# Optimization experiments

Measured on AMD Instinct MI355X. Metric: run time of the kernel, lower is better.

The kernel has to match this reference:

```python
import jax, jax.numpy as jnp
import numpy as np

N = 50000
SELF_LOOP_W = 2.0  # GCNConv(improved=True)


def gcn_conv(x, edge_index, W, b):
    # x: [N, Fin], edge_index: [2, E] (row=source, col=target)
    h = x @ W  # [N, Fout]
    row, col = edge_index[0], edge_index[1]
    ones = jnp.ones(row.shape[0], dtype=h.dtype)
    deg = jax.ops.segment_sum(ones, col, num_segments=N) + SELF_LOOP_W
    dinv = jnp.where(deg > 0, jax.lax.rsqrt(deg), 0.0)
    norm = dinv[row] * dinv[col]  # [E]
    agg = jax.ops.segment_sum(norm[:, None] * h[row], col, num_segments=N)
    # self-loop contribution: weight 2.0, norm = dinv[i]^2
    agg = agg + (SELF_LOOP_W * dinv * dinv)[:, None] * h
    return agg + b


def setup_inputs() -> dict:
    key = jax.random.key(0)
    ks = jax.random.split(key, 12)
    F_in, H1, H2, H3 = 256, 256, 128, 64
    E, Ep, En = 800000, 200000, 200000
    def glorot(k, shape):
        lim = np.sqrt(6.0 / (shape[0] + shape[1]))
        return jax.random.uniform(k, shape, jnp.float32, -lim, lim)
    return {
        "x": jax.random.normal(ks[0], (N, F_in), jnp.float32),
        "train_edge_index": jax.random.randint(ks[1], (2, E), 0, N),
        "pos_edge_index": jax.random.randint(ks[2], (2, Ep), 0, N),
        "neg_edge_index": jax.random.randint(ks[3], (2, En), 0, N),
        "W1": glorot(ks[4], (F_in, H1)),
        "b1": jnp.zeros((H1,), jnp.float32),
        "W2": glorot(ks[5], (H1, H2)),
        "b2": jnp.zeros((H2,), jnp.float32),
        "Wl1": glorot(ks[6], (H2, H3)),
        "bl1": jnp.zeros((H3,), jnp.float32),
        "Wl2": glorot(ks[7], (H3, 1)),
        "bl2": jnp.zeros((1,), jnp.float32),
    }


def reference(x, train_edge_index, pos_edge_index, neg_edge_index,
              W1, b1, W2, b2, Wl1, bl1, Wl2, bl2):
    h = jax.nn.relu(gcn_conv(x, train_edge_index, W1, b1))
    h = gcn_conv(h, train_edge_index, W2, b2)  # [N, 128]
    tei = jnp.concatenate([pos_edge_index, neg_edge_index], axis=-1)  # [2, Ep+En]
    e = h[tei[1]] + h[tei[0]]  # x_i + x_j, [Etot, 128]
    e = jax.nn.relu(e @ Wl1 + bl1)
    e = jax.nn.sigmoid(e @ Wl2 + bl2)
    return e.reshape(-1)
```

## Files before the change

### kernel.cpp

```cpp
#include <hip/hip_runtime.h>
#include <math.h>

#define NV 50000
#define ETR 800000
#define EPOS 200000
#define ETEST 400000

typedef __attribute__((ext_vector_type(8))) short bf16x8;
typedef __attribute__((ext_vector_type(8))) unsigned short ushortx8;
typedef __attribute__((ext_vector_type(4))) float f32x4;

__device__ inline unsigned short f2b(float f) {
    union { float f; unsigned u; } v; v.f = f;
    unsigned r = v.u + 0x7fffu + ((v.u >> 16) & 1u);
    return (unsigned short)(r >> 16);
}
__device__ inline float blo(unsigned q) { union { unsigned u; float f; } v; v.u = q << 16; return v.f; }
__device__ inline float bhi(unsigned q) { union { unsigned u; float f; } v; v.u = q & 0xffff0000u; return v.f; }
__device__ inline float b2f(unsigned short s) { union { unsigned u; float f; } v; v.u = ((unsigned)s) << 16; return v.f; }

#define GLOAD_LDS16(g, l) __builtin_amdgcn_global_load_lds( \
    (__attribute__((address_space(1))) void*)(g), \
    (__attribute__((address_space(3))) void*)(l), 16, 0, 0)


template<int N, int K, bool AF32, int NCOLS = N>
__device__ __forceinline__ void gemm_body(
    const void* __restrict__ Av, const unsigned short* __restrict__ Bt,
    unsigned short* __restrict__ C, int M, int row0, int col0)
{
    constexpr int BK = 64;
    __shared__ unsigned short smem[18464];
    unsigned short (*Asm)[BK] = (unsigned short (*)[BK])smem;
    unsigned short (*Bsm)[BK] = (unsigned short (*)[BK])(smem + 8192);
    int tid = threadIdx.x;
    int lane = tid & 63, wid = tid >> 6;
    int wr = wid >> 1, wc = wid & 1;

    int sr = tid >> 3;
    int s8 = tid & 7;
    int fr = lane & 15;
    int g  = lane >> 4;

    f32x4 acc[4][4] = {};

    for (int k0 = 0; k0 < K; k0 += BK) {
        #pragma unroll
        for (int i = 0; i < 4; ++i) {
            int r = sr + i * 32;
            int gr = row0 + r;
            int s8sw = s8 ^ (r & 7);
            GLOAD_LDS16(&Bt[(size_t)(col0 + r) * K + k0 + s8sw * 8], &Bsm[r][s8 * 8]);
            if constexpr (AF32) {
                const float* Af = (const float*)Av;
                ushortx8 va = {0, 0, 0, 0, 0, 0, 0, 0};
                if (gr < M) {
                    float4 f0 = *(const float4*)&Af[(size_t)gr * K + k0 + s8 * 8];
                    float4 f1 = *(const float4*)&Af[(size_t)gr * K + k0 + s8 * 8 + 4];
                    va[0] = f2b(f0.x); va[1] = f2b(f0.y); va[2] = f2b(f0.z); va[3] = f2b(f0.w);
                    va[4] = f2b(f1.x); va[5] = f2b(f1.y); va[6] = f2b(f1.z); va[7] = f2b(f1.w);
                }
                *(ushortx8*)&Asm[r][(s8 ^ (r & 7)) * 8] = va;
            } else {
                const unsigned short* Ab = (const unsigned short*)Av;
                GLOAD_LDS16(&Ab[(size_t)gr * K + k0 + s8sw * 8], &Asm[r][s8 * 8]);
            }
        }
        __syncthreads();
        #pragma unroll
        for (int kf = 0; kf < BK; kf += 32) {
            int sbase = kf >> 3;
            bf16x8 af[4], bfr[4];
            #pragma unroll
            for (int m = 0; m < 4; ++m) {
                int rr = wr * 64 + m * 16 + fr;
                af[m] = *(const bf16x8*)&Asm[rr][((sbase + g) ^ (fr & 7)) * 8];
            }
            #pragma unroll
            for (int n = 0; n < 4; ++n) {
                int rr = wc * 64 + n * 16 + fr;
                bfr[n] = *(const bf16x8*)&Bsm[rr][((sbase + g) ^ (fr & 7)) * 8];
            }
            #pragma unroll
            for (int m = 0; m < 4; ++m)
                #pragma unroll
                for (int n = 0; n < 4; ++n)
                    acc[m][n] = __builtin_amdgcn_mfma_f32_16x16x32_bf16(af[m], bfr[n], acc[m][n], 0, 0, 0);
        }
        __syncthreads();
    }

    {
        unsigned short* cw = smem + wid * 4616;
        #pragma unroll
        for (int m = 0; m < 4; ++m)
            #pragma unroll
            for (int n = 0; n < 4; ++n)
                #pragma unroll
                for (int j = 0; j < 4; ++j)
                    cw[(m * 16 + g * 4 + j) * 72 + n * 16 + fr] = f2b(acc[m][n][j]);
        __syncthreads();
        int row = tid >> 1;
        int half = tid & 1;
        int q = ((row >> 6) << 1) + half;
        int rl = row & 63;
        const unsigned short* cr = smem + q * 4616 + rl * 72;
        int gr = row0 + row;
        if (gr < M && half * 64 < NCOLS) {
            unsigned short* gp = C + (size_t)gr * NCOLS + col0 + half * 64;
            #pragma unroll
            for (int c8 = 0; c8 < 8; ++c8)
                *(ushortx8*)&gp[c8 * 8] = *(const ushortx8*)&cr[c8 * 8];
        }
    }
}


__global__ __launch_bounds__(256) void fat0_kernel(
    const int* __restrict__ tei, int* __restrict__ deg,
    const float* __restrict__ W1, unsigned short* __restrict__ w1t)
{
    int bid = blockIdx.x;
    int t = threadIdx.x;
    if (bid < 3125) {
        int e = bid * 256 + t;
        if (e < ETR) atomicAdd(&deg[tei[ETR + e]], 1);
    } else {
        int i = (bid - 3125) * 256 + t;
        w1t[i] = f2b(W1[(i & 255) * 256 + (i >> 8)]);
    }
}


__global__ __launch_bounds__(1024) void ptr2_kernel(
    const int* __restrict__ deg, int* __restrict__ ptr,
    int* __restrict__ cursor, float* __restrict__ dinv)
{
    int b = blockIdx.x, t = threadIdx.x;
    int lane = t & 63, w = t >> 6;
    __shared__ int wred[16], wsum[16], woff[16];
    __shared__ int base_s;

    int pre = 0;
    int lim = b * 1024;
    for (int i = t; i < lim; i += 1024) pre += deg[i];
    #pragma unroll
    for (int off = 32; off > 0; off >>= 1) pre += __shfl_xor(pre, off);
    if (lane == 0) wred[w] = pre;
    __syncthreads();
    if (t == 0) {
        int s = 0;
        #pragma unroll
        for (int k = 0; k < 16; ++k) s += wred[k];
        base_s = s;
    }

    int i = b * 1024 + t;
    int d = (i < NV) ? deg[i] : 0;
    int v = d;
    #pragma unroll
    for (int off = 1; off < 64; off <<= 1) {
        int u = __shfl_up(v, off);
        if (lane >= off) v += u;
    }
    if (lane == 63) wsum[w] = v;
    __syncthreads();
    if (t == 0) {
        int s = base_s;
        #pragma unroll
        for (int k = 0; k < 16; ++k) { woff[k] = s; s += wsum[k]; }
    }
    __syncthreads();
    int excl = woff[w] + v - d;
    if (i < NV) {
        ptr[i] = excl;
        cursor[i] = excl;
        dinv[i] = rsqrtf((float)d + 2.0f);
        if (i == NV - 1) ptr[NV] = excl + d;
    }
}


__global__ __launch_bounds__(256) void fat1_kernel(
    const float* __restrict__ x, const unsigned short* __restrict__ w1t,
    unsigned short* __restrict__ h1lin,
    const int* __restrict__ tei, const float* __restrict__ dinv,
    int* __restrict__ cursor, int2* __restrict__ edat,
    const float* __restrict__ W2, unsigned short* __restrict__ w2t,
    const float* __restrict__ Wl1, unsigned short* __restrict__ wl1t)
{
    int bid = blockIdx.x;
    int t = threadIdx.x;
    if (bid < 782) {
        int row0 = (bid >> 1) * 128, col0 = (bid & 1) * 128;
        gemm_body<256, 256, true>(x, w1t, h1lin, NV, row0, col0);
    } else if (bid < 3907) {
        int e = (bid - 782) * 256 + t;
        if (e < ETR) {
            int row = tei[e];
            int col = tei[ETR + e];
            int p = atomicAdd(&cursor[col], 1);
            edat[p] = make_int2(row, __float_as_int(dinv[row] * dinv[col]));
        }
    } else if (bid < 4035) {
        int i = (bid - 3907) * 256 + t;
        w2t[i] = f2b(W2[(i & 255) * 128 + (i >> 8)]);
    } else if (bid < 4067) {
        int i = (bid - 4035) * 256 + t;
        wl1t[i] = f2b(Wl1[(i & 127) * 64 + (i >> 7)]);
    } else {
        int i = (bid - 4067) * 256 + t;
        wl1t[8192 + i] = 0;
    }
}


__global__ __launch_bounds__(256) void gemm2_kernel(
    const unsigned short* __restrict__ A, const unsigned short* __restrict__ Bt,
    unsigned short* __restrict__ C)
{
    gemm_body<128, 256, false>(A, Bt, C, NV, blockIdx.x * 128, 0);
}

__global__ __launch_bounds__(256) void gemm_u_kernel(
    const unsigned short* __restrict__ A, const unsigned short* __restrict__ Bt,
    unsigned short* __restrict__ C)
{
    gemm_body<128, 128, false, 64>(A, Bt, C, NV, blockIdx.x * 128, 0);
}


template<int F, bool RELU>
__global__ __launch_bounds__(256) void gather_kernel(
    const int* __restrict__ ptr, const int2* __restrict__ edat,
    const float* __restrict__ dinv, const unsigned short* __restrict__ hlin,
    const float* __restrict__ bias, unsigned short* __restrict__ hout)
{
    constexpr int V = F / 64;
    int gid = blockIdx.x * blockDim.x + threadIdx.x;
    int node = gid >> 6, lane = gid & 63;
    if (node >= NV) return;
    float dc = dinv[node];
    int j0 = ptr[node], j1 = ptr[node + 1];
    float acc[V] = {};
    const unsigned short* hb = hlin + lane * V;
    const long long* edl = (const long long*)edat;

    int j = j0;
    for (; j + 7 < j1; j += 8) {
        long long e[8];
        #pragma unroll
        for (int u = 0; u < 8; ++u) e[u] = __builtin_nontemporal_load(edl + j + u);
        if constexpr (V == 4) {
            uint2 q[8];
            #pragma unroll
            for (int u = 0; u < 8; ++u)
                q[u] = *(const uint2*)(hb + (size_t)(int)e[u] * F);
            #pragma unroll
            for (int u = 0; u < 8; ++u) {
                float n = __int_as_float((int)(e[u] >> 32));
                acc[0] += n * blo(q[u].x);
                acc[1] += n * bhi(q[u].x);
                acc[2] += n * blo(q[u].y);
                acc[3] += n * bhi(q[u].y);
            }
        } else {
            unsigned q[8];
            #pragma unroll
            for (int u = 0; u < 8; ++u)
                q[u] = *(const unsigned*)(hb + (size_t)(int)e[u] * F);
            #pragma unroll
            for (int u = 0; u < 8; ++u) {
                float n = __int_as_float((int)(e[u] >> 32));
                acc[0] += n * blo(q[u]);
                acc[1] += n * bhi(q[u]);
            }
        }
    }
    for (; j + 3 < j1; j += 4) {
        long long e[4];
        #pragma unroll
        for (int u = 0; u < 4; ++u) e[u] = __builtin_nontemporal_load(edl + j + u);
        if constexpr (V == 4) {
            uint2 q[4];
            #pragma unroll
            for (int u = 0; u < 4; ++u)
                q[u] = *(const uint2*)(hb + (size_t)(int)e[u] * F);
            #pragma unroll
            for (int u = 0; u < 4; ++u) {
                float n = __int_as_float((int)(e[u] >> 32));
                acc[0] += n * blo(q[u].x);
                acc[1] += n * bhi(q[u].x);
                acc[2] += n * blo(q[u].y);
                acc[3] += n * bhi(q[u].y);
            }
        } else {
            unsigned q[4];
            #pragma unroll
            for (int u = 0; u < 4; ++u)
                q[u] = *(const unsigned*)(hb + (size_t)(int)e[u] * F);
            #pragma unroll
            for (int u = 0; u < 4; ++u) {
                float n = __int_as_float((int)(e[u] >> 32));
                acc[0] += n * blo(q[u]);
                acc[1] += n * bhi(q[u]);
            }
        }
    }
    for (; j < j1; ++j) {
        long long e0 = __builtin_nontemporal_load(edl + j);
        float n0 = __int_as_float((int)(e0 >> 32));
        if constexpr (V == 4) {
            uint2 q0 = *(const uint2*)(hb + (size_t)(int)e0 * F);
            acc[0] += n0 * blo(q0.x);
            acc[1] += n0 * bhi(q0.x);
            acc[2] += n0 * blo(q0.y);
            acc[3] += n0 * bhi(q0.y);
        } else {
            unsigned q0 = *(const unsigned*)(hb + (size_t)(int)e0 * F);
            acc[0] += n0 * blo(q0);
            acc[1] += n0 * bhi(q0);
        }
    }

    const unsigned short* ps = hb + (size_t)node * F;
    float sw = 2.0f * dc * dc;
    if constexpr (V == 4) {
        uint2 qs = *(const uint2*)ps;
        float o0 = acc[0] + sw * blo(qs.x) + bias[lane * 4 + 0];
        float o1 = acc[1] + sw * bhi(qs.x) + bias[lane * 4 + 1];
        float o2 = acc[2] + sw * blo(qs.y) + bias[lane * 4 + 2];
        float o3 = acc[3] + sw * bhi(qs.y) + bias[lane * 4 + 3];
        if (RELU) {
            o0 = fmaxf(o0, 0.f); o1 = fmaxf(o1, 0.f);
            o2 = fmaxf(o2, 0.f); o3 = fmaxf(o3, 0.f);
        }
        union { unsigned short u[4]; unsigned long long ll; } pk;
        pk.u[0] = f2b(o0); pk.u[1] = f2b(o1); pk.u[2] = f2b(o2); pk.u[3] = f2b(o3);
        __builtin_nontemporal_store(pk.ll, (unsigned long long*)(hout + (size_t)node * F + lane * 4));
    } else {
        unsigned qs = *(const unsigned*)ps;
        float o0 = acc[0] + sw * blo(qs) + bias[lane * 2 + 0];
        float o1 = acc[1] + sw * bhi(qs) + bias[lane * 2 + 1];
        if (RELU) { o0 = fmaxf(o0, 0.f); o1 = fmaxf(o1, 0.f); }
        union { unsigned short u[2]; unsigned q; } pk;
        pk.u[0] = f2b(o0); pk.u[1] = f2b(o1);
        __builtin_nontemporal_store(pk.q, (unsigned*)(hout + (size_t)node * F + lane * 2));
    }
}


__global__ __launch_bounds__(256) void edge_head_kernel(
    const int* __restrict__ pos, const int* __restrict__ neg,
    const unsigned short* __restrict__ u,
    const float* __restrict__ bl1, const float* __restrict__ Wl2,
    const float* __restrict__ bl2, float* __restrict__ out)
{
    int tid = threadIdx.x;
    int wv = tid >> 6, lane = tid & 63;
    int sub = lane >> 4, fl = lane & 15;
    int e = blockIdx.x * 16 + wv * 4 + sub;
    if (e >= ETEST) return;
    int a, b;
    if (e < EPOS) { a = pos[e]; b = pos[EPOS + e]; }
    else { int i = e - EPOS; a = neg[i]; b = neg[EPOS + i]; }
    uint2 qa = *(const uint2*)&u[(size_t)a * 64 + fl * 4];
    uint2 qb = *(const uint2*)&u[(size_t)b * 64 + fl * 4];
    float4 b1 = *(const float4*)&bl1[fl * 4];
    float4 w2 = *(const float4*)&Wl2[fl * 4];
    float s = fmaxf(blo(qa.x) + blo(qb.x) + b1.x, 0.f) * w2.x
            + fmaxf(bhi(qa.x) + bhi(qb.x) + b1.y, 0.f) * w2.y
            + fmaxf(blo(qa.y) + blo(qb.y) + b1.z, 0.f) * w2.z
            + fmaxf(bhi(qa.y) + bhi(qb.y) + b1.w, 0.f) * w2.w;
    #pragma unroll
    for (int off = 8; off > 0; off >>= 1)
        s += __shfl_xor(s, off);
    if (fl == 0)
        out[e] = 1.0f / (1.0f + expf(-(s + bl2[0])));
}


extern "C" void kernel_launch(void* const* d_in, const int* in_sizes, int n_in,
                              void* d_out, int out_size, void* d_ws, size_t ws_size,
                              hipStream_t stream) {
    const float* x   = (const float*)d_in[0];
    const int*   tei = (const int*)d_in[1];
    const int*   pos = (const int*)d_in[2];
    const int*   neg = (const int*)d_in[3];
    const float* W1  = (const float*)d_in[4];
    const float* b1  = (const float*)d_in[5];
    const float* W2  = (const float*)d_in[6];
    const float* b2  = (const float*)d_in[7];
    const float* Wl1 = (const float*)d_in[8];
    const float* bl1 = (const float*)d_in[9];
    const float* Wl2 = (const float*)d_in[10];
    const float* bl2 = (const float*)d_in[11];
    float* out = (float*)d_out;

    float* fws = (float*)d_ws;
    int*   iws = (int*)d_ws;
    unsigned short* usws = (unsigned short*)d_ws;
    float* dinv     = fws;
    int*   deg      = iws + 50000;
    int*   ptr      = iws + 100000;
    int*   cursor   = iws + 150002;
    int2*  edat     = (int2*)(iws + 200064);
    unsigned short* w1t  = usws + 2ull * 1800192;
    unsigned short* w2t  = usws + 2ull * 1832960;
    unsigned short* bufX = usws + 2ull * 1853504;
    unsigned short* bufL16 = usws + 2ull * 8253504;
    unsigned short* bufH = usws + 2ull * 14653504;
    unsigned short* wl1t = usws + 2ull * 21053504;
    unsigned short* ubuf = usws + 2ull * 21061696;

    hipMemsetAsync(deg, 0, NV * sizeof(int), stream);

    fat0_kernel<<<3381, 256, 0, stream>>>(tei, deg, W1, w1t);

    ptr2_kernel<<<49, 1024, 0, stream>>>(deg, ptr, cursor, dinv);

    fat1_kernel<<<4099, 256, 0, stream>>>(x, w1t, bufL16, tei, dinv, cursor, edat,
                                          W2, w2t, Wl1, wl1t);

    gather_kernel<256, true><<<(NV * 64) / 256, 256, 0, stream>>>(ptr, edat, dinv, bufL16, b1, bufH);

    gemm2_kernel<<<391, 256, 0, stream>>>(bufH, w2t, bufX);
    gather_kernel<128, false><<<(NV * 64) / 256, 256, 0, stream>>>(ptr, edat, dinv, bufX, b2, bufL16);

    gemm_u_kernel<<<391, 256, 0, stream>>>(bufL16, wl1t, ubuf);
    edge_head_kernel<<<ETEST / 16, 256, 0, stream>>>(pos, neg, ubuf, bl1, Wl2, bl2, out);
}
```

Baseline: 262.8 us.

## Fold W2 and Wl1 into one weight so layer-2 aggregation runs at width 64

```diff
diff --git a/kernel.cpp b/kernel.cpp
--- a/kernel.cpp
+++ b/kernel.cpp
@@ -118,16 +118,37 @@
 
 __global__ __launch_bounds__(256) void fat0_kernel(
     const int* __restrict__ tei, int* __restrict__ deg,
-    const float* __restrict__ W1, unsigned short* __restrict__ w1t)
+    const float* __restrict__ W1, unsigned short* __restrict__ w1t,
+    const float* __restrict__ W2, const float* __restrict__ Wl1,
+    const float* __restrict__ b2, unsigned short* __restrict__ wct,
+    float* __restrict__ c2f)
 {
     int bid = blockIdx.x;
     int t = threadIdx.x;
     if (bid < 3125) {
         int e = bid * 256 + t;
         if (e < ETR) atomicAdd(&deg[tei[ETR + e]], 1);
-    } else {
+    } else if (bid < 3381) {
         int i = (bid - 3125) * 256 + t;
         w1t[i] = f2b(W1[(i & 255) * 256 + (i >> 8)]);
+    } else if (bid < 3509) {
+        int n = bid - 3381;
+        int k = t;
+        if (n < 64) {
+            float s = 0.f;
+            for (int j = 0; j < 128; ++j)
+                s += W2[k * 128 + j] * Wl1[j * 64 + n];
+            wct[n * 256 + k] = f2b(s);
+        } else {
+            wct[n * 256 + k] = 0;
+        }
+    } else {
+        if (t < 64) {
+            float s = 0.f;
+            for (int j = 0; j < 128; ++j)
+                s += b2[j] * Wl1[j * 64 + t];
+            c2f[t] = s;
+        }
     }
 }
 
@@ -185,16 +206,14 @@
     const float* __restrict__ x, const unsigned short* __restrict__ w1t,
     unsigned short* __restrict__ h1lin,
     const int* __restrict__ tei, const float* __restrict__ dinv,
-    int* __restrict__ cursor, int2* __restrict__ edat,
-    const float* __restrict__ W2, unsigned short* __restrict__ w2t,
-    const float* __restrict__ Wl1, unsigned short* __restrict__ wl1t)
+    int* __restrict__ cursor, int2* __restrict__ edat)
 {
     int bid = blockIdx.x;
     int t = threadIdx.x;
     if (bid < 782) {
         int row0 = (bid >> 1) * 128, col0 = (bid & 1) * 128;
         gemm_body<256, 256, true>(x, w1t, h1lin, NV, row0, col0);
-    } else if (bid < 3907) {
+    } else {
         int e = (bid - 782) * 256 + t;
         if (e < ETR) {
             int row = tei[e];
@@ -202,31 +221,15 @@
             int p = atomicAdd(&cursor[col], 1);
             edat[p] = make_int2(row, __float_as_int(dinv[row] * dinv[col]));
         }
-    } else if (bid < 4035) {
-        int i = (bid - 3907) * 256 + t;
-        w2t[i] = f2b(W2[(i & 255) * 128 + (i >> 8)]);
-    } else if (bid < 4067) {
-        int i = (bid - 4035) * 256 + t;
-        wl1t[i] = f2b(Wl1[(i & 127) * 64 + (i >> 7)]);
-    } else {
-        int i = (bid - 4067) * 256 + t;
-        wl1t[8192 + i] = 0;
-    }
-}
-
-
-__global__ __launch_bounds__(256) void gemm2_kernel(
+    }
+}
+
+
+__global__ __launch_bounds__(256) void gemm_v_kernel(
     const unsigned short* __restrict__ A, const unsigned short* __restrict__ Bt,
     unsigned short* __restrict__ C)
 {
-    gemm_body<128, 256, false>(A, Bt, C, NV, blockIdx.x * 128, 0);
-}
-
-__global__ __launch_bounds__(256) void gemm_u_kernel(
-    const unsigned short* __restrict__ A, const unsigned short* __restrict__ Bt,
-    unsigned short* __restrict__ C)
-{
-    gemm_body<128, 128, false, 64>(A, Bt, C, NV, blockIdx.x * 128, 0);
+    gemm_body<128, 256, false, 64>(A, Bt, C, NV, blockIdx.x * 128, 0);
 }
 
 
@@ -265,15 +268,14 @@
                 acc[3] += n * bhi(q[u].y);
             }
         } else {
-            unsigned q[8];
+            unsigned short q[8];
             #pragma unroll
             for (int u = 0; u < 8; ++u)
-                q[u] = *(const unsigned*)(hb + (size_t)(int)e[u] * F);
+                q[u] = hb[(size_t)(int)e[u] * F];
             #pragma unroll
             for (int u = 0; u < 8; ++u) {
                 float n = __int_as_float((int)(e[u] >> 32));
-                acc[0] += n * blo(q[u]);
-                acc[1] += n * bhi(q[u]);
+                acc[0] += n * b2f(q[u]);
             }
         }
     }
@@ -295,15 +297,14 @@
                 acc[3] += n * bhi(q[u].y);
             }
         } else {
-            unsigned q[4];
+            unsigned short q[4];
             #pragma unroll
             for (int u = 0; u < 4; ++u)
-                q[u] = *(const unsigned*)(hb + (size_t)(int)e[u] * F);
+                q[u] = hb[(size_t)(int)e[u] * F];
             #pragma unroll
             for (int u = 0; u < 4; ++u) {
                 float n = __int_as_float((int)(e[u] >> 32));
-                acc[0] += n * blo(q[u]);
-                acc[1] += n * bhi(q[u]);
+                acc[0] += n * b2f(q[u]);
             }
         }
     }
@@ -317,9 +318,7 @@
             acc[2] += n0 * blo(q0.y);
             acc[3] += n0 * bhi(q0.y);
         } else {
-            unsigned q0 = *(const unsigned*)(hb + (size_t)(int)e0 * F);
-            acc[0] += n0 * blo(q0);
-            acc[1] += n0 * bhi(q0);
+            acc[0] += n0 * b2f(hb[(size_t)(int)e0 * F]);
         }
     }
 
@@ -339,13 +338,9 @@
         pk.u[0] = f2b(o0); pk.u[1] = f2b(o1); pk.u[2] = f2b(o2); pk.u[3] = f2b(o3);
         __builtin_nontemporal_store(pk.ll, (unsigned long long*)(hout + (size_t)node * F + lane * 4));
     } else {
-        unsigned qs = *(const unsigned*)ps;
-        float o0 = acc[0] + sw * blo(qs) + bias[lane * 2 + 0];
-        float o1 = acc[1] + sw * bhi(qs) + bias[lane * 2 + 1];
-        if (RELU) { o0 = fmaxf(o0, 0.f); o1 = fmaxf(o1, 0.f); }
-        union { unsigned short u[2]; unsigned q; } pk;
-        pk.u[0] = f2b(o0); pk.u[1] = f2b(o1);
-        __builtin_nontemporal_store(pk.q, (unsigned*)(hout + (size_t)node * F + lane * 2));
+        float o0 = acc[0] + sw * b2f(*ps) + bias[lane];
+        if (RELU) o0 = fmaxf(o0, 0.f);
+        __builtin_nontemporal_store((unsigned short)f2b(o0), hout + (size_t)node * F + lane);
     }
 }
 
@@ -406,27 +401,25 @@
     int*   cursor   = iws + 150002;
     int2*  edat     = (int2*)(iws + 200064);
     unsigned short* w1t  = usws + 2ull * 1800192;
-    unsigned short* w2t  = usws + 2ull * 1832960;
-    unsigned short* bufX = usws + 2ull * 1853504;
-    unsigned short* bufL16 = usws + 2ull * 8253504;
-    unsigned short* bufH = usws + 2ull * 14653504;
-    unsigned short* wl1t = usws + 2ull * 21053504;
-    unsigned short* ubuf = usws + 2ull * 21061696;
+    unsigned short* wct  = usws + 2ull * 1832960;
+    float* c2f      = fws + 1849344;
+    unsigned short* bufL16 = usws + 2ull * 1853504;
+    unsigned short* bufH   = usws + 2ull * 8253504;
+    unsigned short* vbuf   = usws + 2ull * 14653504;
+    unsigned short* ubuf   = usws + 2ull * 16253504;
 
     hipMemsetAsync(deg, 0, NV * sizeof(int), stream);
 
-    fat0_kernel<<<3381, 256, 0, stream>>>(tei, deg, W1, w1t);
+    fat0_kernel<<<3510, 256, 0, stream>>>(tei, deg, W1, w1t, W2, Wl1, b2, wct, c2f);
 
     ptr2_kernel<<<49, 1024, 0, stream>>>(deg, ptr, cursor, dinv);
 
-    fat1_kernel<<<4099, 256, 0, stream>>>(x, w1t, bufL16, tei, dinv, cursor, edat,
-                                          W2, w2t, Wl1, wl1t);
+    fat1_kernel<<<3907, 256, 0, stream>>>(x, w1t, bufL16, tei, dinv, cursor, edat);
 
     gather_kernel<256, true><<<(NV * 64) / 256, 256, 0, stream>>>(ptr, edat, dinv, bufL16, b1, bufH);
 
-    gemm2_kernel<<<391, 256, 0, stream>>>(bufH, w2t, bufX);
-    gather_kernel<128, false><<<(NV * 64) / 256, 256, 0, stream>>>(ptr, edat, dinv, bufX, b2, bufL16);
-
-    gemm_u_kernel<<<391, 256, 0, stream>>>(bufL16, wl1t, ubuf);
+    gemm_v_kernel<<<391, 256, 0, stream>>>(bufH, wct, vbuf);
+    gather_kernel<64, false><<<(NV * 64) / 256, 256, 0, stream>>>(ptr, edat, dinv, vbuf, c2f, ubuf);
+
     edge_head_kernel<<<ETEST / 16, 256, 0, stream>>>(pos, neg, ubuf, bl1, Wl2, bl2, out);
 }
```

Result: faster. 254.6 us (-3.1%).
